# Kernel optimization log

Hardware: AMD Instinct MI355X
Metric: run time of the kernel (lower is better)

The kernel has to match this reference:

```python
import jax, jax.numpy as jnp
import numpy as np

DIM, HEADS, WIN = 256, 8, 8
HD = DIM // HEADS
SCALE = HD ** -0.5


def _rel_index(w):
    # Swin-style relative position index, computed statically in numpy
    coords = np.stack(np.meshgrid(np.arange(w), np.arange(w), indexing='ij'))  # (2,w,w)
    cf = coords.reshape(2, -1)                      # (2, w*w)
    rel = (cf[:, :, None] - cf[:, None, :]).transpose(1, 2, 0)  # (w*w, w*w, 2)
    rel = rel.copy()
    rel[:, :, 0] += w - 1
    rel[:, :, 1] += w - 1
    rel[:, :, 0] *= 2 * w - 1
    return rel.sum(-1)                              # (w*w, w*w)

REL_IDX = _rel_index(WIN)


def setup_inputs() -> dict:
    key = jax.random.key(0)
    ks = jax.random.split(key, 6)
    B, C, D, H, W = 8, DIM, 100, WIN, WIN
    return {
        'x': jax.random.normal(ks[0], (B, C, D, H, W), jnp.float32),
        'dwconv_w': jax.random.normal(ks[1], (C, C, 1, 3, 3), jnp.float32) * 0.02,
        'dwconv_b': jnp.zeros((C,), jnp.float32),
        'qkv_w': jax.random.normal(ks[2], (3 * C, C), jnp.float32) * 0.02,
        'qkv_b': jnp.zeros((3 * C,), jnp.float32),
        'proj_w': jax.random.normal(ks[3], (C, C), jnp.float32) * 0.02,
        'proj_b': jnp.zeros((C,), jnp.float32),
        'rpb_table': jax.random.normal(ks[4], ((2 * WIN - 1) ** 2, HEADS), jnp.float32) * 0.02,
    }


def reference(x, dwconv_w, dwconv_b, qkv_w, qkv_b, proj_w, proj_b, rpb_table):
    B, C, D, H, W = x.shape
    N = H * W
    # 'dwconv': full Conv3d, kernel (1,3,3), padding (0,1,1)
    xl = jax.lax.conv_general_dilated(
        x, dwconv_w, window_strides=(1, 1, 1),
        padding=[(0, 0), (1, 1), (1, 1)],
        dimension_numbers=('NCDHW', 'OIDHW', 'NCDHW'),
    ) + dwconv_b[None, :, None, None, None]
    # qkv: 1x1x1 conv == pointwise linear over channels
    qkv = jnp.einsum('oc,bcdhw->bodhw', qkv_w, xl) + qkv_b[None, :, None, None, None]
    # channel dim layout: (three, head, head_dim)
    qkv = qkv.reshape(B, 3, HEADS, HD, D, N)
    q, k, v = qkv[:, 0], qkv[:, 1], qkv[:, 2]      # each (B, HEADS, HD, D, N)
    attn = jnp.einsum('bhcdn,bhcdm->bdhnm', q * SCALE, k)  # (B, D, HEADS, N, N)
    bias = rpb_table[REL_IDX.reshape(-1)].reshape(N, N, HEADS).transpose(2, 0, 1)
    attn = jax.nn.softmax(attn + bias[None, None], axis=-1)
    xa = jnp.einsum('bdhnm,bhcdm->bhcdn', attn, v)  # (B, HEADS, HD, D, N)
    xa = xa.reshape(B, C, D, H, W)                  # channel = (head, head_dim)
    out = jnp.einsum('oc,bcdhw->bodhw', proj_w, xa) + proj_b[None, :, None, None, None]
    return out
```

## Files before the change

kernel.cpp:

```cpp
#include <hip/hip_runtime.h>
#include <cstdint>
#include <cstddef>

#define SCALEQ 0.17677669529663689f

typedef _Float16 half_t;
typedef _Float16 half8   __attribute__((ext_vector_type(8)));
typedef _Float16 half4v  __attribute__((ext_vector_type(4)));
typedef float    float4v __attribute__((ext_vector_type(4)));

#define GLDS16(gp, lp)                                                        \
  __builtin_amdgcn_global_load_lds(                                           \
      (const __attribute__((address_space(1))) void*)(gp),                    \
      (__attribute__((address_space(3))) void*)(lp), 16, 0, 0)

__global__ __launch_bounds__(256) void prep_all(
    const float* __restrict__ x, const float* __restrict__ dwconv_w,
    const float* __restrict__ qkv_w, const float* __restrict__ proj_w,
    const float* __restrict__ rpb, half_t* __restrict__ xpad,
    half_t* __restrict__ Wt, half_t* __restrict__ qw16,
    half_t* __restrict__ pw16, float* __restrict__ btab) {
  __shared__ float tile[128 * 65];
  const int blk = blockIdx.x, t = threadIdx.x;
  if (blk < 800) {
    const int bd = blk, b = bd / 100, d = bd % 100;
    for (int hf = 0; hf < 2; ++hf) {
      for (int i = 0; i < 32; ++i) {
        int idx = i * 256 + t, c = idx >> 6, hw = idx & 63;
        tile[c * 65 + hw] = x[(size_t)((b * 256 + hf * 128 + c) * 100 + d) * 64 + hw];
      }
      __syncthreads();
      for (int i = 0; i < 50; ++i) {
        int idx = i * 256 + t, cell = idx >> 7, c = idx & 127;
        int hh = cell / 10, ww = cell % 10;
        float v = 0.f;
        if (hh >= 1 && hh <= 8 && ww >= 1 && ww <= 8)
          v = tile[c * 65 + (hh - 1) * 8 + (ww - 1)];
        xpad[(size_t)(bd * 100 + cell) * 256 + hf * 128 + c] = (half_t)v;
      }
      __syncthreads();
    }
  } else if (blk < 944) {
    const int base = (blk - 800) * 4096;
#pragma unroll
    for (int i = 0; i < 16; ++i) {
      int idx = base + i * 256 + t;
      int tap = idx >> 16, rem = idx & 65535;
      int o = rem >> 8, c = rem & 255;
      Wt[idx] = (half_t)dwconv_w[(o * 256 + c) * 9 + tap];
    }
  } else if (blk < 1040) {
    const int base = (blk - 944) * 2048;
#pragma unroll
    for (int i = 0; i < 8; ++i) {
      int idx = base + i * 256 + t;
      float v = qkv_w[idx];
      if (idx < 65536) v *= SCALEQ;
      qw16[idx] = (half_t)v;
    }
  } else if (blk < 1072) {
    const int base = (blk - 1040) * 2048;
#pragma unroll
    for (int i = 0; i < 8; ++i) {
      int idx = base + i * 256 + t;
      pw16[idx] = (half_t)proj_w[idx];
    }
  } else {
    const int base = (blk - 1072) * 2048;
#pragma unroll
    for (int i = 0; i < 8; ++i) {
      int idx = base + i * 256 + t;
      int hd = idx >> 12, n = (idx >> 6) & 63, m = idx & 63;
      int h1 = n >> 3, w1 = n & 7, h2 = m >> 3, w2 = m & 7;
      int ridx = (h1 - h2 + 7) * 15 + (w1 - w2 + 7);
      btab[idx] = rpb[ridx * 8 + hd];
    }
  }
}

__global__ __launch_bounds__(256) void conv_kernel(
    const half_t* __restrict__ Wt, const half_t* __restrict__ xpad,
    const float* __restrict__ convb, half_t* __restrict__ xl) {
  __shared__ __align__(16) half_t Asm[128 * 64];
  __shared__ __align__(16) half_t Bsm[128 * 64];
  const int blk = blockIdx.x;
  const int o0 = (blk & 1) * 128;
  const int n0 = (blk >> 1) * 128;
  const int tid = threadIdx.x;
  const int wave = tid >> 6, lane = tid & 63;
  const int l15 = lane & 15, quad = lane >> 4;
  const int wm = wave >> 1, wn = wave & 1;
  const int srow = tid >> 3;
  const int cg = (tid & 7) ^ (srow & 7);

  int pixbase[4], arow[4];
#pragma unroll
  for (int i = 0; i < 4; ++i) {
    int P = n0 + srow + i * 32;
    int bd = P >> 6, hw = P & 63;
    pixbase[i] = (bd * 100 + (hw >> 3) * 10 + (hw & 7)) * 512 + cg * 16;
    arow[i] = (o0 + srow + i * 32) * 512 + cg * 16;
  }

  float4v acc[4][4];
#pragma unroll
  for (int mi = 0; mi < 4; ++mi)
#pragma unroll
    for (int ni = 0; ni < 4; ++ni) {
      float4v z = {0.f, 0.f, 0.f, 0.f};
      acc[mi][ni] = z;
    }

  const char* xpc = (const char*)xpad;
  for (int tap = 0; tap < 9; ++tap) {
    const char* wt = (const char*)Wt + tap * 131072;
    const int toff = ((tap / 3) * 10 + (tap % 3)) * 512;
    for (int c0 = 0; c0 < 512; c0 += 128) {
#pragma unroll
      for (int i = 0; i < 4; ++i) {
        GLDS16(wt + arow[i] + c0, (char*)Asm + i * 4096 + wave * 1024);
        GLDS16(xpc + pixbase[i] + toff + c0, (char*)Bsm + i * 4096 + wave * 1024);
      }
      __syncthreads();
#pragma unroll
      for (int kh = 0; kh < 2; ++kh) {
        half8 af[4], bf[4];
#pragma unroll
        for (int mi = 0; mi < 4; ++mi) {
          int r = wm * 64 + mi * 16 + l15;
          af[mi] = *(const half8*)&Asm[r * 64 + (((kh * 4 + quad) ^ (r & 7)) * 8)];
        }
#pragma unroll
        for (int ni = 0; ni < 4; ++ni) {
          int r = wn * 64 + ni * 16 + l15;
          bf[ni] = *(const half8*)&Bsm[r * 64 + (((kh * 4 + quad) ^ (r & 7)) * 8)];
        }
#pragma unroll
        for (int mi = 0; mi < 4; ++mi)
#pragma unroll
          for (int ni = 0; ni < 4; ++ni)
            acc[mi][ni] = __builtin_amdgcn_mfma_f32_16x16x32_f16(
                af[mi], bf[ni], acc[mi][ni], 0, 0, 0);
      }
      __syncthreads();
    }
  }
#pragma unroll
  for (int mi = 0; mi < 4; ++mi) {
    const int o4 = o0 + wm * 64 + mi * 16 + quad * 4;
    const float b0 = convb[o4], b1 = convb[o4 + 1], b2 = convb[o4 + 2], b3 = convb[o4 + 3];
#pragma unroll
    for (int ni = 0; ni < 4; ++ni) {
      const int P = n0 + wn * 64 + ni * 16 + l15;
      half4v h;
      h.x = (half_t)(acc[mi][ni].x + b0);
      h.y = (half_t)(acc[mi][ni].y + b1);
      h.z = (half_t)(acc[mi][ni].z + b2);
      h.w = (half_t)(acc[mi][ni].w + b3);
      *(half4v*)(xl + (size_t)P * 256 + o4) = h;
    }
  }
}

__global__ __launch_bounds__(512) void fused_tail2(
    const half_t* __restrict__ xlg, const half_t* __restrict__ qw,
    const float* __restrict__ qkvb, const float* __restrict__ btab,
    const half_t* __restrict__ pw, const float* __restrict__ projb,
    float* __restrict__ out32) {
  __shared__ __align__(16) half_t LS[78336];
  const int bd = blockIdx.x;
  const int tid = threadIdx.x;
  const int wave = tid >> 6, lane = tid & 63;
  const int l15 = lane & 15, quad = lane >> 4;
  const int head = wave;

  half_t* xlp = LS;
  half_t* xa = LS;
  float* T = (float*)LS;
  half_t* scr = LS + 16896 + wave * 7680;
  half_t* qsc = scr;
  half_t* ksc = scr + 2560;
  half_t* vsc = scr + 5120;
  half_t* Psc = scr;

  {
    const char* src = (const char*)(xlg + (size_t)bd * 64 * 256);
#pragma unroll
    for (int i = 0; i < 4; ++i) {
      int row = i * 16 + wave * 2 + (lane >> 5);
      int sch = (lane & 31) ^ (row & 7);
      GLDS16(src + row * 512 + sch * 16, (char*)xlp + (i * 16 + wave * 2) * 512);
    }
  }
  __syncthreads();

  for (int p = 0; p < 2; ++p) {
    const half_t* Wp = qw + p * 65536 + head * 32 * 256;
    float4v acc[2][4];
#pragma unroll
    for (int mi = 0; mi < 2; ++mi)
#pragma unroll
      for (int ni = 0; ni < 4; ++ni) {
        float4v z = {0.f, 0.f, 0.f, 0.f};
        acc[mi][ni] = z;
      }
#pragma unroll
    for (int kh = 0; kh < 8; ++kh) {
      half8 af[2], bf[4];
#pragma unroll
      for (int mi = 0; mi < 2; ++mi)
        af[mi] = *(const half8*)(Wp + (mi * 16 + l15) * 256 + kh * 32 + quad * 8);
#pragma unroll
      for (int ni = 0; ni < 4; ++ni) {
        int r = ni * 16 + l15;
        bf[ni] = *(const half8*)&xlp[r * 256 + (((kh * 4 + quad) ^ (r & 7)) * 8)];
      }
#pragma unroll
      for (int mi = 0; mi < 2; ++mi)
#pragma unroll
        for (int ni = 0; ni < 4; ++ni)
          acc[mi][ni] = __builtin_amdgcn_mfma_f32_16x16x32_f16(
              af[mi], bf[ni], acc[mi][ni], 0, 0, 0);
    }
    half_t* dst = (p == 0) ? qsc : ksc;
    const float sc = (p == 0) ? SCALEQ : 1.0f;
#pragma unroll
    for (int mi = 0; mi < 2; ++mi) {
      const float4v b4 = *(const float4v*)&qkvb[p * 256 + head * 32 + mi * 16 + quad * 4];
#pragma unroll
      for (int ni = 0; ni < 4; ++ni) {
        half4v h;
        h.x = (half_t)(acc[mi][ni].x + b4.x * sc);
        h.y = (half_t)(acc[mi][ni].y + b4.y * sc);
        h.z = (half_t)(acc[mi][ni].z + b4.z * sc);
        h.w = (half_t)(acc[mi][ni].w + b4.w * sc);
        *(half4v*)(dst + (ni * 16 + l15) * 40 + mi * 16 + quad * 4) = h;
      }
    }
  }

  {
    const half_t* Wp = qw + 2 * 65536 + head * 32 * 256;
    float4v acc[2][4];
#pragma unroll
    for (int mi = 0; mi < 2; ++mi)
#pragma unroll
      for (int ni = 0; ni < 4; ++ni) {
        float4v z = {0.f, 0.f, 0.f, 0.f};
        acc[mi][ni] = z;
      }
#pragma unroll
    for (int kh = 0; kh < 8; ++kh) {
      half8 af[2], bf[4];
#pragma unroll
      for (int mi = 0; mi < 2; ++mi)
        af[mi] = *(const half8*)(Wp + (mi * 16 + l15) * 256 + kh * 32 + quad * 8);
#pragma unroll
      for (int ni = 0; ni < 4; ++ni) {
        int r = ni * 16 + l15;
        bf[ni] = *(const half8*)&xlp[r * 256 + (((kh * 4 + quad) ^ (r & 7)) * 8)];
      }
#pragma unroll
      for (int mi = 0; mi < 2; ++mi)
#pragma unroll
        for (int ni = 0; ni < 4; ++ni)
          acc[mi][ni] = __builtin_amdgcn_mfma_f32_16x16x32_f16(
              af[mi], bf[ni], acc[mi][ni], 0, 0, 0);
    }
#pragma unroll
    for (int mi = 0; mi < 2; ++mi) {
      const float4v b4 = *(const float4v*)&qkvb[512 + head * 32 + mi * 16 + quad * 4];
#pragma unroll
      for (int ni = 0; ni < 4; ++ni) {
#pragma unroll
        for (int iv = 0; iv < 4; ++iv)
          vsc[(mi * 16 + quad * 4 + iv) * 72 + ni * 16 + l15] =
              (half_t)(acc[mi][ni][iv] + b4[iv]);
      }
    }
  }

  __builtin_amdgcn_s_waitcnt(0);

  half8 aq[4], bk[4];
#pragma unroll
  for (int i = 0; i < 4; ++i) {
    aq[i] = *(const half8*)(qsc + (i * 16 + l15) * 40 + quad * 8);
    bk[i] = *(const half8*)(ksc + (i * 16 + l15) * 40 + quad * 8);
  }
  float4v s[4][4];
#pragma unroll
  for (int ni = 0; ni < 4; ++ni)
#pragma unroll
    for (int mi = 0; mi < 4; ++mi) {
      float4v z = {0.f, 0.f, 0.f, 0.f};
      s[ni][mi] = __builtin_amdgcn_mfma_f32_16x16x32_f16(aq[ni], bk[mi], z, 0, 0, 0);
    }
  const float* bh = btab + head * 4096;
#pragma unroll
  for (int ni = 0; ni < 4; ++ni)
#pragma unroll
    for (int i = 0; i < 4; ++i) {
      const int n = ni * 16 + quad * 4 + i;
#pragma unroll
      for (int mi = 0; mi < 4; ++mi) s[ni][mi][i] += bh[n * 64 + mi * 16 + l15];
    }
  float inv[4][4];
#pragma unroll
  for (int ni = 0; ni < 4; ++ni)
#pragma unroll
    for (int i = 0; i < 4; ++i) {
      float mx = fmaxf(fmaxf(s[ni][0][i], s[ni][1][i]), fmaxf(s[ni][2][i], s[ni][3][i]));
      for (int off = 1; off < 16; off <<= 1) mx = fmaxf(mx, __shfl_xor(mx, off));
      float sum = 0.f;
#pragma unroll
      for (int mi = 0; mi < 4; ++mi) {
        float e = __expf(s[ni][mi][i] - mx);
        s[ni][mi][i] = e;
        sum += e;
      }
      for (int off = 1; off < 16; off <<= 1) sum += __shfl_xor(sum, off);
      inv[ni][i] = 1.0f / sum;
    }
#pragma unroll
  for (int ni = 0; ni < 4; ++ni)
#pragma unroll
    for (int i = 0; i < 4; ++i) {
      const int n = ni * 16 + quad * 4 + i;
#pragma unroll
      for (int mi = 0; mi < 4; ++mi)
        Psc[n * 72 + mi * 16 + l15] = (half_t)(s[ni][mi][i] * inv[ni][i]);
    }
  __builtin_amdgcn_s_waitcnt(0);

  half8 av[2][2];
#pragma unroll
  for (int ci = 0; ci < 2; ++ci)
#pragma unroll
    for (int k2 = 0; k2 < 2; ++k2)
      av[ci][k2] = *(const half8*)(vsc + (ci * 16 + l15) * 72 + k2 * 32 + quad * 8);
  float4v oa[2][4];
#pragma unroll
  for (int ci = 0; ci < 2; ++ci)
#pragma unroll
    for (int ni = 0; ni < 4; ++ni) {
      float4v z = {0.f, 0.f, 0.f, 0.f};
      oa[ci][ni] = z;
    }
#pragma unroll
  for (int ni = 0; ni < 4; ++ni)
#pragma unroll
    for (int k2 = 0; k2 < 2; ++k2) {
      half8 bp = *(const half8*)&Psc[(ni * 16 + l15) * 72 + k2 * 32 + quad * 8];
#pragma unroll
      for (int ci = 0; ci < 2; ++ci)
        oa[ci][ni] = __builtin_amdgcn_mfma_f32_16x16x32_f16(av[ci][k2], bp, oa[ci][ni], 0, 0, 0);
    }

  __syncthreads();

#pragma unroll
  for (int ci = 0; ci < 2; ++ci)
#pragma unroll
    for (int ni = 0; ni < 4; ++ni) {
      half4v h = {(half_t)oa[ci][ni].x, (half_t)oa[ci][ni].y,
                  (half_t)oa[ci][ni].z, (half_t)oa[ci][ni].w};
      *(half4v*)(xa + (ni * 16 + l15) * 264 + head * 32 + ci * 16 + quad * 4) = h;
    }
  __syncthreads();

  float4v pacc[2][4];
#pragma unroll
  for (int mi = 0; mi < 2; ++mi)
#pragma unroll
    for (int ni = 0; ni < 4; ++ni) {
      float4v z = {0.f, 0.f, 0.f, 0.f};
      pacc[mi][ni] = z;
    }
#pragma unroll
  for (int kh = 0; kh < 8; ++kh) {
    half8 af[2], bf[4];
#pragma unroll
    for (int mi = 0; mi < 2; ++mi)
      af[mi] = *(const half8*)(pw + (wave * 32 + mi * 16 + l15) * 256 + kh * 32 + quad * 8);
#pragma unroll
    for (int ni = 0; ni < 4; ++ni)
      bf[ni] = *(const half8*)&xa[(ni * 16 + l15) * 264 + kh * 32 + quad * 8];
#pragma unroll
    for (int mi = 0; mi < 2; ++mi)
#pragma unroll
      for (int ni = 0; ni < 4; ++ni)
        pacc[mi][ni] = __builtin_amdgcn_mfma_f32_16x16x32_f16(
            af[mi], bf[ni], pacc[mi][ni], 0, 0, 0);
  }
#pragma unroll
  for (int mi = 0; mi < 2; ++mi) {
    const float4v b4 = *(const float4v*)&projb[wave * 32 + mi * 16 + quad * 4];
#pragma unroll
    for (int ni = 0; ni < 4; ++ni) {
      pacc[mi][ni].x += b4.x;
      pacc[mi][ni].y += b4.y;
      pacc[mi][ni].z += b4.z;
      pacc[mi][ni].w += b4.w;
    }
  }

  const int b = bd / 100, d = bd % 100;
  const size_t bdbase = (size_t)b * 1638400 + (size_t)d * 64;
  const int tr = tid >> 3;
  const int col0 = (tid & 7) * 8;
  for (int r = 0; r < 4; ++r) {
    __syncthreads();
    if ((wave >> 1) == r) {
      const int rb = (wave & 1) * 32;
#pragma unroll
      for (int mi = 0; mi < 2; ++mi)
#pragma unroll
        for (int ni = 0; ni < 4; ++ni)
#pragma unroll
          for (int iv = 0; iv < 4; ++iv)
            T[(rb + mi * 16 + quad * 4 + iv) * 68 + ni * 16 + l15] = pacc[mi][ni][iv];
    }
    __syncthreads();
    const int o = r * 64 + tr;
    float* dst = out32 + bdbase + (size_t)o * 6400 + col0;
    const float* srcT = &T[tr * 68 + col0];
    *(float4v*)dst = *(const float4v*)srcT;
    *(float4v*)(dst + 4) = *(const float4v*)(srcT + 4);
  }
}

extern "C" void kernel_launch(void* const* d_in, const int* in_sizes, int n_in,
                              void* d_out, int out_size, void* d_ws, size_t ws_size,
                              hipStream_t stream) {
  const float* x        = (const float*)d_in[0];
  const float* dwconv_w = (const float*)d_in[1];
  const float* dwconv_b = (const float*)d_in[2];
  const float* qkv_w    = (const float*)d_in[3];
  const float* qkv_b    = (const float*)d_in[4];
  const float* proj_w   = (const float*)d_in[5];
  const float* proj_b   = (const float*)d_in[6];
  const float* rpb      = (const float*)d_in[7];
  float* out = (float*)d_out;

  char* ws = (char*)d_ws;
  size_t off = 0;
  half_t* xpad = (half_t*)(ws + off); off += 40960000;
  half_t* xl   = (half_t*)(ws + off); off += 26214400;
  half_t* Wt   = (half_t*)(ws + off); off += 1179648;
  half_t* qw16 = (half_t*)(ws + off); off += 393216;
  half_t* pw16 = (half_t*)(ws + off); off += 131072;
  float*  btab = (float*)(ws + off);  off += 131072;

  prep_all<<<1088, 256, 0, stream>>>(x, dwconv_w, qkv_w, proj_w, rpb,
                                     xpad, Wt, qw16, pw16, btab);
  conv_kernel<<<800, 256, 0, stream>>>(Wt, xpad, dwconv_b, xl);
  fused_tail2<<<800, 512, 0, stream>>>(xl, qw16, qkv_b, btab, pw16, proj_b, out);
}
```

Before: 302.7 us.

## Split each head across two waves in fused tail kernel with 1024 threads

The fused attention/projection tail kernel now runs 16 waves per block instead of 8. Each head is handled by two waves, each owning half of the 64 window pixels for QKV, softmax and PV, and the projection GEMM is split into 16-row slices per wave. This is meant to raise parallelism and latency hiding per block, since only 800 blocks exist. In exchange it adds block-wide syncs, because waves of the same head now share K/V scratch, and it cuts per-wave MFMA reuse while shrinking LDS scratch slightly.

```diff
diff --git a/kernel.cpp b/kernel.cpp
--- a/kernel.cpp
+++ b/kernel.cpp
@@ -162,22 +162,22 @@
   }
 }
 
-__global__ __launch_bounds__(512) void fused_tail2(
+__global__ __launch_bounds__(1024) void fused_tail5(
     const half_t* __restrict__ xlg, const half_t* __restrict__ qw,
     const float* __restrict__ qkvb, const float* __restrict__ btab,
     const half_t* __restrict__ pw, const float* __restrict__ projb,
     float* __restrict__ out32) {
-  __shared__ __align__(16) half_t LS[78336];
+  __shared__ __align__(16) half_t LS[76288];
   const int bd = blockIdx.x;
   const int tid = threadIdx.x;
   const int wave = tid >> 6, lane = tid & 63;
   const int l15 = lane & 15, quad = lane >> 4;
-  const int head = wave;
+  const int head = wave >> 1, half = wave & 1;
 
   half_t* xlp = LS;
   half_t* xa = LS;
   float* T = (float*)LS;
-  half_t* scr = LS + 16896 + wave * 7680;
+  half_t* scr = LS + 16896 + head * 7424;
   half_t* qsc = scr;
   half_t* ksc = scr + 2560;
   half_t* vsc = scr + 5120;
@@ -186,111 +186,85 @@
   {
     const char* src = (const char*)(xlg + (size_t)bd * 64 * 256);
 #pragma unroll
-    for (int i = 0; i < 4; ++i) {
-      int row = i * 16 + wave * 2 + (lane >> 5);
+    for (int i = 0; i < 2; ++i) {
+      int row = i * 32 + wave * 2 + (lane >> 5);
       int sch = (lane & 31) ^ (row & 7);
-      GLDS16(src + row * 512 + sch * 16, (char*)xlp + (i * 16 + wave * 2) * 512);
+      GLDS16(src + row * 512 + sch * 16, (char*)xlp + (i * 32 + wave * 2) * 512);
     }
   }
   __syncthreads();
 
-  for (int p = 0; p < 2; ++p) {
+  for (int p = 0; p < 3; ++p) {
     const half_t* Wp = qw + p * 65536 + head * 32 * 256;
-    float4v acc[2][4];
+    float4v acc[2][2];
 #pragma unroll
     for (int mi = 0; mi < 2; ++mi)
 #pragma unroll
-      for (int ni = 0; ni < 4; ++ni) {
+      for (int ni = 0; ni < 2; ++ni) {
         float4v z = {0.f, 0.f, 0.f, 0.f};
         acc[mi][ni] = z;
       }
 #pragma unroll
     for (int kh = 0; kh < 8; ++kh) {
-      half8 af[2], bf[4];
+      half8 bf[2], af[2];
+#pragma unroll
+      for (int ni = 0; ni < 2; ++ni) {
+        int r = half * 32 + ni * 16 + l15;
+        bf[ni] = *(const half8*)&xlp[r * 256 + (((kh * 4 + quad) ^ (r & 7)) * 8)];
+      }
 #pragma unroll
       for (int mi = 0; mi < 2; ++mi)
         af[mi] = *(const half8*)(Wp + (mi * 16 + l15) * 256 + kh * 32 + quad * 8);
 #pragma unroll
-      for (int ni = 0; ni < 4; ++ni) {
-        int r = ni * 16 + l15;
-        bf[ni] = *(const half8*)&xlp[r * 256 + (((kh * 4 + quad) ^ (r & 7)) * 8)];
-      }
-#pragma unroll
       for (int mi = 0; mi < 2; ++mi)
 #pragma unroll
-        for (int ni = 0; ni < 4; ++ni)
+        for (int ni = 0; ni < 2; ++ni)
           acc[mi][ni] = __builtin_amdgcn_mfma_f32_16x16x32_f16(
               af[mi], bf[ni], acc[mi][ni], 0, 0, 0);
     }
-    half_t* dst = (p == 0) ? qsc : ksc;
-    const float sc = (p == 0) ? SCALEQ : 1.0f;
-#pragma unroll
-    for (int mi = 0; mi < 2; ++mi) {
-      const float4v b4 = *(const float4v*)&qkvb[p * 256 + head * 32 + mi * 16 + quad * 4];
-#pragma unroll
-      for (int ni = 0; ni < 4; ++ni) {
-        half4v h;
-        h.x = (half_t)(acc[mi][ni].x + b4.x * sc);
-        h.y = (half_t)(acc[mi][ni].y + b4.y * sc);
-        h.z = (half_t)(acc[mi][ni].z + b4.z * sc);
-        h.w = (half_t)(acc[mi][ni].w + b4.w * sc);
-        *(half4v*)(dst + (ni * 16 + l15) * 40 + mi * 16 + quad * 4) = h;
-      }
-    }
-  }
-
-  {
-    const half_t* Wp = qw + 2 * 65536 + head * 32 * 256;
-    float4v acc[2][4];
-#pragma unroll
-    for (int mi = 0; mi < 2; ++mi)
-#pragma unroll
-      for (int ni = 0; ni < 4; ++ni) {
-        float4v z = {0.f, 0.f, 0.f, 0.f};
-        acc[mi][ni] = z;
-      }
-#pragma unroll
-    for (int kh = 0; kh < 8; ++kh) {
-      half8 af[2], bf[4];
-#pragma unroll
-      for (int mi = 0; mi < 2; ++mi)
-        af[mi] = *(const half8*)(Wp + (mi * 16 + l15) * 256 + kh * 32 + quad * 8);
-#pragma unroll
-      for (int ni = 0; ni < 4; ++ni) {
-        int r = ni * 16 + l15;
-        bf[ni] = *(const half8*)&xlp[r * 256 + (((kh * 4 + quad) ^ (r & 7)) * 8)];
-      }
-#pragma unroll
-      for (int mi = 0; mi < 2; ++mi)
-#pragma unroll
-        for (int ni = 0; ni < 4; ++ni)
-          acc[mi][ni] = __builtin_amdgcn_mfma_f32_16x16x32_f16(
-              af[mi], bf[ni], acc[mi][ni], 0, 0, 0);
-    }
-#pragma unroll
-    for (int mi = 0; mi < 2; ++mi) {
-      const float4v b4 = *(const float4v*)&qkvb[512 + head * 32 + mi * 16 + quad * 4];
-#pragma unroll
-      for (int ni = 0; ni < 4; ++ni) {
-#pragma unroll
-        for (int iv = 0; iv < 4; ++iv)
-          vsc[(mi * 16 + quad * 4 + iv) * 72 + ni * 16 + l15] =
-              (half_t)(acc[mi][ni][iv] + b4[iv]);
-      }
-    }
-  }
-
-  __builtin_amdgcn_s_waitcnt(0);
-
-  half8 aq[4], bk[4];
-#pragma unroll
-  for (int i = 0; i < 4; ++i) {
-    aq[i] = *(const half8*)(qsc + (i * 16 + l15) * 40 + quad * 8);
+    if (p < 2) {
+      half_t* dst = (p == 0) ? qsc : ksc;
+      const float sc = (p == 0) ? SCALEQ : 1.0f;
+#pragma unroll
+      for (int mi = 0; mi < 2; ++mi) {
+        const float4v b4 = *(const float4v*)&qkvb[p * 256 + head * 32 + mi * 16 + quad * 4];
+#pragma unroll
+        for (int ni = 0; ni < 2; ++ni) {
+          const int px = half * 32 + ni * 16 + l15;
+          half4v h;
+          h.x = (half_t)(acc[mi][ni].x + b4.x * sc);
+          h.y = (half_t)(acc[mi][ni].y + b4.y * sc);
+          h.z = (half_t)(acc[mi][ni].z + b4.z * sc);
+          h.w = (half_t)(acc[mi][ni].w + b4.w * sc);
+          *(half4v*)(dst + px * 40 + mi * 16 + quad * 4) = h;
+        }
+      }
+    } else {
+#pragma unroll
+      for (int mi = 0; mi < 2; ++mi) {
+        const float4v b4 = *(const float4v*)&qkvb[512 + head * 32 + mi * 16 + quad * 4];
+#pragma unroll
+        for (int ni = 0; ni < 2; ++ni) {
+          const int px = half * 32 + ni * 16 + l15;
+#pragma unroll
+          for (int iv = 0; iv < 4; ++iv)
+            vsc[(mi * 16 + quad * 4 + iv) * 72 + px] = (half_t)(acc[mi][ni][iv] + b4[iv]);
+        }
+      }
+    }
+  }
+  __syncthreads();
+
+  half8 aq[2], bk[4];
+#pragma unroll
+  for (int i = 0; i < 2; ++i)
+    aq[i] = *(const half8*)(qsc + (half * 32 + i * 16 + l15) * 40 + quad * 8);
+#pragma unroll
+  for (int i = 0; i < 4; ++i)
     bk[i] = *(const half8*)(ksc + (i * 16 + l15) * 40 + quad * 8);
-  }
-  float4v s[4][4];
-#pragma unroll
-  for (int ni = 0; ni < 4; ++ni)
+  float4v s[2][4];
+#pragma unroll
+  for (int ni = 0; ni < 2; ++ni)
 #pragma unroll
     for (int mi = 0; mi < 4; ++mi) {
       float4v z = {0.f, 0.f, 0.f, 0.f};
@@ -298,16 +272,16 @@
     }
   const float* bh = btab + head * 4096;
 #pragma unroll
-  for (int ni = 0; ni < 4; ++ni)
+  for (int ni = 0; ni < 2; ++ni)
 #pragma unroll
     for (int i = 0; i < 4; ++i) {
-      const int n = ni * 16 + quad * 4 + i;
+      const int n = half * 32 + ni * 16 + quad * 4 + i;
 #pragma unroll
       for (int mi = 0; mi < 4; ++mi) s[ni][mi][i] += bh[n * 64 + mi * 16 + l15];
     }
-  float inv[4][4];
-#pragma unroll
-  for (int ni = 0; ni < 4; ++ni)
+  float inv[2][4];
+#pragma unroll
+  for (int ni = 0; ni < 2; ++ni)
 #pragma unroll
     for (int i = 0; i < 4; ++i) {
       float mx = fmaxf(fmaxf(s[ni][0][i], s[ni][1][i]), fmaxf(s[ni][2][i], s[ni][3][i]));
@@ -322,11 +296,13 @@
       for (int off = 1; off < 16; off <<= 1) sum += __shfl_xor(sum, off);
       inv[ni][i] = 1.0f / sum;
     }
-#pragma unroll
-  for (int ni = 0; ni < 4; ++ni)
+  __syncthreads();
+
+#pragma unroll
+  for (int ni = 0; ni < 2; ++ni)
 #pragma unroll
     for (int i = 0; i < 4; ++i) {
-      const int n = ni * 16 + quad * 4 + i;
+      const int n = half * 32 + ni * 16 + quad * 4 + i;
 #pragma unroll
       for (int mi = 0; mi < 4; ++mi)
         Psc[n * 72 + mi * 16 + l15] = (half_t)(s[ni][mi][i] * inv[ni][i]);
@@ -339,94 +315,81 @@
 #pragma unroll
     for (int k2 = 0; k2 < 2; ++k2)
       av[ci][k2] = *(const half8*)(vsc + (ci * 16 + l15) * 72 + k2 * 32 + quad * 8);
-  float4v oa[2][4];
+  float4v oa[2][2];
 #pragma unroll
   for (int ci = 0; ci < 2; ++ci)
 #pragma unroll
-    for (int ni = 0; ni < 4; ++ni) {
+    for (int ni = 0; ni < 2; ++ni) {
       float4v z = {0.f, 0.f, 0.f, 0.f};
       oa[ci][ni] = z;
     }
 #pragma unroll
-  for (int ni = 0; ni < 4; ++ni)
+  for (int ni = 0; ni < 2; ++ni)
 #pragma unroll
     for (int k2 = 0; k2 < 2; ++k2) {
-      half8 bp = *(const half8*)&Psc[(ni * 16 + l15) * 72 + k2 * 32 + quad * 8];
+      half8 bp = *(const half8*)&Psc[(half * 32 + ni * 16 + l15) * 72 + k2 * 32 + quad * 8];
 #pragma unroll
       for (int ci = 0; ci < 2; ++ci)
         oa[ci][ni] = __builtin_amdgcn_mfma_f32_16x16x32_f16(av[ci][k2], bp, oa[ci][ni], 0, 0, 0);
     }
 
-  __syncthreads();
-
 #pragma unroll
   for (int ci = 0; ci < 2; ++ci)
 #pragma unroll
-    for (int ni = 0; ni < 4; ++ni) {
+    for (int ni = 0; ni < 2; ++ni) {
+      const int px = half * 32 + ni * 16 + l15;
       half4v h = {(half_t)oa[ci][ni].x, (half_t)oa[ci][ni].y,
                   (half_t)oa[ci][ni].z, (half_t)oa[ci][ni].w};
-      *(half4v*)(xa + (ni * 16 + l15) * 264 + head * 32 + ci * 16 + quad * 4) = h;
+      *(half4v*)(xa + px * 264 + head * 32 + ci * 16 + quad * 4) = h;
     }
   __syncthreads();
 
-  float4v pacc[2][4];
-#pragma unroll
-  for (int mi = 0; mi < 2; ++mi)
-#pragma unroll
-    for (int ni = 0; ni < 4; ++ni) {
-      float4v z = {0.f, 0.f, 0.f, 0.f};
-      pacc[mi][ni] = z;
-    }
+  float4v pacc[4];
+#pragma unroll
+  for (int ni = 0; ni < 4; ++ni) {
+    float4v z = {0.f, 0.f, 0.f, 0.f};
+    pacc[ni] = z;
+  }
 #pragma unroll
   for (int kh = 0; kh < 8; ++kh) {
-    half8 af[2], bf[4];
-#pragma unroll
-    for (int mi = 0; mi < 2; ++mi)
-      af[mi] = *(const half8*)(pw + (wave * 32 + mi * 16 + l15) * 256 + kh * 32 + quad * 8);
+    half8 af = *(const half8*)(pw + (wave * 16 + l15) * 256 + kh * 32 + quad * 8);
+    half8 bf[4];
 #pragma unroll
     for (int ni = 0; ni < 4; ++ni)
       bf[ni] = *(const half8*)&xa[(ni * 16 + l15) * 264 + kh * 32 + quad * 8];
 #pragma unroll
-    for (int mi = 0; mi < 2; ++mi)
-#pragma unroll
-      for (int ni = 0; ni < 4; ++ni)
-        pacc[mi][ni] = __builtin_amdgcn_mfma_f32_16x16x32_f16(
-            af[mi], bf[ni], pacc[mi][ni], 0, 0, 0);
-  }
-#pragma unroll
-  for (int mi = 0; mi < 2; ++mi) {
-    const float4v b4 = *(const float4v*)&projb[wave * 32 + mi * 16 + quad * 4];
+    for (int ni = 0; ni < 4; ++ni)
+      pacc[ni] = __builtin_amdgcn_mfma_f32_16x16x32_f16(af, bf[ni], pacc[ni], 0, 0, 0);
+  }
+  {
+    const float4v b4 = *(const float4v*)&projb[wave * 16 + quad * 4];
 #pragma unroll
     for (int ni = 0; ni < 4; ++ni) {
-      pacc[mi][ni].x += b4.x;
-      pacc[mi][ni].y += b4.y;
-      pacc[mi][ni].z += b4.z;
-      pacc[mi][ni].w += b4.w;
+      pacc[ni].x += b4.x;
+      pacc[ni].y += b4.y;
+      pacc[ni].z += b4.z;
+      pacc[ni].w += b4.w;
     }
   }
 
   const int b = bd / 100, d = bd % 100;
   const size_t bdbase = (size_t)b * 1638400 + (size_t)d * 64;
-  const int tr = tid >> 3;
-  const int col0 = (tid & 7) * 8;
+  const int tr = tid >> 4;
+  const int col0 = (tid & 15) * 4;
   for (int r = 0; r < 4; ++r) {
     __syncthreads();
-    if ((wave >> 1) == r) {
-      const int rb = (wave & 1) * 32;
-#pragma unroll
-      for (int mi = 0; mi < 2; ++mi)
-#pragma unroll
-        for (int ni = 0; ni < 4; ++ni)
-#pragma unroll
-          for (int iv = 0; iv < 4; ++iv)
-            T[(rb + mi * 16 + quad * 4 + iv) * 68 + ni * 16 + l15] = pacc[mi][ni][iv];
+    if ((wave >> 2) == r) {
+      const int rb = (wave & 3) * 16;
+#pragma unroll
+      for (int ni = 0; ni < 4; ++ni)
+#pragma unroll
+        for (int iv = 0; iv < 4; ++iv)
+          T[(rb + quad * 4 + iv) * 68 + ni * 16 + l15] = pacc[ni][iv];
     }
     __syncthreads();
     const int o = r * 64 + tr;
-    float* dst = out32 + bdbase + (size_t)o * 6400 + col0;
-    const float* srcT = &T[tr * 68 + col0];
-    *(float4v*)dst = *(const float4v*)srcT;
-    *(float4v*)(dst + 4) = *(const float4v*)(srcT + 4);
+    *(float4v*)(out32 + bdbase + (size_t)o * 6400 + col0) =
+        *(const float4v*)&T[tr * 68 + col0];
   }
 }
 
@@ -455,5 +418,5 @@
   prep_all<<<1088, 256, 0, stream>>>(x, dwconv_w, qkv_w, proj_w, rpb,
                                      xpad, Wt, qw16, pw16, btab);
   conv_kernel<<<800, 256, 0, stream>>>(Wt, xpad, dwconv_b, xl);
-  fused_tail2<<<800, 512, 0, stream>>>(xl, qw16, qkv_b, btab, pw16, proj_b, out);
+  fused_tail5<<<800, 1024, 0, stream>>>(xl, qw16, qkv_b, btab, pw16, proj_b, out);
 }
```

After: 335.1 us. 1.11x slower.
